# Optimization experiments

Hardware: AMD Instinct MI355X
Metric: run time of the kernel (lower is better)

## Reference

```python
import jax, jax.numpy as jnp
import numpy as np

ALPHA = 0.2  # leaky relu slope
NEG = -9e15


def setup_inputs() -> dict:
    key = jax.random.key(0)
    k1, k2, k3, k4 = jax.random.split(key, 4)
    B, N, Fin, Fout = 16, 2048, 256, 256
    h = jax.random.normal(k1, (B, N, Fin), dtype=jnp.float32)
    adj = jax.random.randint(k2, (B, N, N), 0, 2, dtype=jnp.int32)
    # xavier_uniform with gain 1.414 on [B, Fin, Fout] (fan over last two dims)
    limW = 1.414 * np.sqrt(6.0 / (Fin + Fout))
    W = jax.random.uniform(k3, (B, Fin, Fout), minval=-limW, maxval=limW, dtype=jnp.float32)
    lima = 1.414 * np.sqrt(6.0 / (2 * Fout + 1))
    a = jax.random.uniform(k4, (B, 2 * Fout, 1), minval=-lima, maxval=lima, dtype=jnp.float32)
    return {"h": h, "adj": adj, "W": W, "a": a}


def reference(h, adj, W, a):
    Fout = W.shape[-1]
    Wh = jnp.einsum('bnf,bfo->bno', h, W)                 # [B,N,Fout]
    Wh1 = jnp.einsum('bno,bo->bn', Wh, a[:, :Fout, 0])    # [B,N]
    Wh2 = jnp.einsum('bno,bo->bn', Wh, a[:, Fout:, 0])    # [B,N]
    e = Wh1[:, :, None] + Wh2[:, None, :]                 # [B,N,N]
    e = jnp.where(e > 0, e, ALPHA * e)                    # leaky relu
    att = jnp.where(adj > 0, e, NEG)
    att = jax.nn.softmax(att, axis=1)                     # NOTE: dim=1 as in source
    # dropout: eval mode -> identity
    h_prime = jnp.einsum('bij,bjo->bio', att, Wh)         # [B,N,Fout]
    return jax.nn.elu(h_prime)                            # concat=True
```

## Files before the change

kernel.cpp:

```cpp
#include <hip/hip_runtime.h>
#include <hip/hip_bf16.h>

typedef unsigned short u16;
typedef unsigned long long u64;
typedef __attribute__((ext_vector_type(8))) short bf16x8;
typedef __attribute__((ext_vector_type(4))) float f32x4;

#define NB 16
#define NN 2048
#define FF 256
#define LOG2E 1.4426950408889634f

__device__ __forceinline__ u16 f2bf(float x) {
    union { float f; unsigned u; } v; v.f = x;
    unsigned r = v.u + 0x7fffu + ((v.u >> 16) & 1u);
    return (u16)(r >> 16);
}

#define GLD_LDS(g, l) __builtin_amdgcn_global_load_lds((const __attribute__((address_space(1))) void*)(g), (__attribute__((address_space(3))) void*)(l), 16, 0, 0)

__global__ __launch_bounds__(256) void k_prep_w(const float* __restrict__ W, const float* __restrict__ a,
                                                u16* __restrict__ WT, float* __restrict__ u1, float* __restrict__ u2) {
    int b = blockIdx.y, t = threadIdx.x;
    __shared__ float a1s[FF], a2s[FF];
    a1s[t] = a[b*2*FF + t];
    a2s[t] = a[b*2*FF + FF + t];
    __syncthreads();
    int f = blockIdx.x*64 + (t >> 2);
    int o0 = (t & 3) * 64;
    const float* wrow = W + (size_t)(b*FF + f)*FF + o0;
    u16* wtb = WT + (size_t)b*FF*FF;
    float s1 = 0.f, s2 = 0.f;
#pragma unroll
    for (int c = 0; c < 16; ++c) {
        float4 v = *(const float4*)(wrow + c*4);
        int o = o0 + c*4;
        s1 += v.x*a1s[o] + v.y*a1s[o+1] + v.z*a1s[o+2] + v.w*a1s[o+3];
        s2 += v.x*a2s[o] + v.y*a2s[o+1] + v.z*a2s[o+2] + v.w*a2s[o+3];
        wtb[(size_t)(o+0)*FF + f] = f2bf(v.x);
        wtb[(size_t)(o+1)*FF + f] = f2bf(v.y);
        wtb[(size_t)(o+2)*FF + f] = f2bf(v.z);
        wtb[(size_t)(o+3)*FF + f] = f2bf(v.w);
    }
    s1 += __shfl_xor(s1, 1); s1 += __shfl_xor(s1, 2);
    s2 += __shfl_xor(s2, 1); s2 += __shfl_xor(s2, 2);
    if ((t & 3) == 0) { u1[b*FF + f] = s1; u2[b*FF + f] = s2; }
}

__global__ __launch_bounds__(256) void k_wh(const float* __restrict__ h, const u16* __restrict__ WT,
                                            const float* __restrict__ u1, const float* __restrict__ u2,
                                            u16* __restrict__ WhT, float* __restrict__ Wh1, float* __restrict__ Wh2) {
    int bid = blockIdx.x;
    int nid = (bid & 7)*64 + (bid >> 3);
    int b  = nid >> 5;
    int i0 = (nid & 31) * 64;
    int t = threadIdx.x, lane = t & 63, wave = t >> 6;
    __shared__ alignas(16) u16 At[256*64];
    __shared__ alignas(16) u16 Bt[64*64];
    __shared__ float u1s[FF], u2s[FF];
    u1s[t] = u1[b*FF + t];
    u2s[t] = u2[b*FF + t];

    const u16*   WTb = WT + (size_t)b*FF*FF;
    const float* hb  = h + ((size_t)b*NN + i0)*FF;
    int r = t >> 2, q = t & 3, kq = q*16;

    f32x4 acc[4][4];
#pragma unroll
    for (int x = 0; x < 4; ++x)
#pragma unroll
        for (int y = 0; y < 4; ++y) acc[x][y] = (f32x4)0.f;
    float s1 = 0.f, s2 = 0.f;
    __syncthreads();

#pragma unroll 1
    for (int kk = 0; kk < 4; ++kk) {
        int k0 = kk*64;
#pragma unroll
        for (int is = 0; is < 8; ++is) {
            int s = is*256 + t;
            int row = s >> 3, jbp = s & 7;
            int jbl = jbp ^ (row & 7);
            GLD_LDS(WTb + (size_t)row*FF + k0 + jbl*8, &At[s*8]);
        }
        {
            const float* hp = hb + (size_t)r*FF + k0 + kq;
            float4 f0 = *(const float4*)(hp + 0);
            float4 f1 = *(const float4*)(hp + 4);
            float4 f2 = *(const float4*)(hp + 8);
            float4 f3 = *(const float4*)(hp + 12);
            float fv[16] = {f0.x,f0.y,f0.z,f0.w, f1.x,f1.y,f1.z,f1.w,
                            f2.x,f2.y,f2.z,f2.w, f3.x,f3.y,f3.z,f3.w};
            union { u16 u[16]; bf16x8 v[2]; } cv;
#pragma unroll
            for (int e = 0; e < 16; ++e) {
                int kidx = k0 + kq + e;
                s1 += fv[e]*u1s[kidx];
                s2 += fv[e]*u2s[kidx];
                cv.u[e] = f2bf(fv[e]);
            }
            int rx = r & 7;
            *(bf16x8*)&Bt[r*64 + ((q*2 + 0) ^ rx)*8] = cv.v[0];
            *(bf16x8*)&Bt[r*64 + ((q*2 + 1) ^ rx)*8] = cv.v[1];
        }
        __syncthreads();
#pragma unroll
        for (int kc = 0; kc < 2; ++kc) {
            int jl = kc*4 + (lane >> 4);
            bf16x8 af[4], bfr[4];
#pragma unroll
            for (int mi = 0; mi < 4; ++mi) {
                int rr2 = wave*64 + mi*16 + (lane & 15);
                af[mi] = *(const bf16x8*)&At[rr2*64 + ((jl ^ (rr2 & 7))*8)];
            }
#pragma unroll
            for (int ni = 0; ni < 4; ++ni) {
                int rr2 = ni*16 + (lane & 15);
                bfr[ni] = *(const bf16x8*)&Bt[rr2*64 + ((jl ^ (rr2 & 7))*8)];
            }
#pragma unroll
            for (int mi = 0; mi < 4; ++mi)
#pragma unroll
                for (int ni = 0; ni < 4; ++ni)
                    acc[mi][ni] = __builtin_amdgcn_mfma_f32_16x16x32_bf16(af[mi], bfr[ni], acc[mi][ni], 0, 0, 0);
        }
        __syncthreads();
    }
    s1 += __shfl_xor(s1, 1); s1 += __shfl_xor(s1, 2);
    s2 += __shfl_xor(s2, 1); s2 += __shfl_xor(s2, 2);
    if (q == 0) { Wh1[b*NN + i0 + r] = s1*LOG2E; Wh2[b*NN + i0 + r] = s2*LOG2E; }

    u16* Wo = WhT + (size_t)b*FF*NN;
#pragma unroll
    for (int mi = 0; mi < 4; ++mi)
#pragma unroll
        for (int ni = 0; ni < 4; ++ni) {
            int i = i0 + ni*16 + (lane & 15);
#pragma unroll
            for (int rr = 0; rr < 4; ++rr) {
                int o = wave*64 + mi*16 + (lane >> 4)*4 + rr;
                Wo[(size_t)o*NN + i] = f2bf(acc[mi][ni][rr]);
            }
        }
}

__global__ __launch_bounds__(256) void k_colsum(const int* __restrict__ adj, const float* __restrict__ Wh1,
                                                const float* __restrict__ Wh2, float* __restrict__ pS,
                                                u64* __restrict__ packed) {
    int b = blockIdx.z, ic = blockIdx.y, jt = blockIdx.x;
    int t = threadIdx.x, lane = t & 63, wave = t >> 6;
    __shared__ float wh1s[128];
    int ibase = ic*128;
    if (t < 128) wh1s[t] = Wh1[b*NN + ibase + t];
    __syncthreads();
    int j = jt*256 + wave*16 + (lane & 15) + (lane >> 4)*64;
    float wh2j = Wh2[b*NN + j];
    const int* acol = adj + (size_t)b*NN*NN + (size_t)ibase*NN + j;
    u64* prow = packed + ((size_t)(b*NN + ibase))*32 + wave*8 + jt;
    float s = 0.f;
#pragma unroll 1
    for (int ii = 0; ii < 128; ii += 16) {
        int v[16];
#pragma unroll
        for (int rr = 0; rr < 16; ++rr) v[rr] = acol[(size_t)(ii + rr)*NN];
#pragma unroll
        for (int rr = 0; rr < 16; ++rr) {
            bool p = v[rr] > 0;
            u64 m = __ballot(p);
            if (lane == 0) prow[(size_t)(ii + rr)*32] = m;
            float tt = wh1s[ii + rr] + wh2j;
            float lr = fmaxf(tt, 0.2f*tt);
            float e = __builtin_amdgcn_exp2f(lr);
            s += p ? e : 0.f;
        }
    }
    pS[((size_t)(b*16 + ic))*NN + j] = s;
}

__global__ __launch_bounds__(512, 1) void k_gemm3(const u16* __restrict__ WhT, const u64* __restrict__ packed,
                                                  const float* __restrict__ Wh1, const float* __restrict__ Wh2,
                                                  const float* __restrict__ pS, float* __restrict__ out) {
    int bid = blockIdx.x;
    int nid = (bid & 7)*32 + (bid >> 3);
    int b  = nid >> 4;
    int i0 = (nid & 15) * 128;
    int t = threadIdx.x, lane = t & 63, wave = t >> 6;
    int wm = wave >> 2, wn = wave & 3;
    __shared__ alignas(16) u16 At[2][128*64];
    __shared__ alignas(16) u16 Bt[3][256*64];
    __shared__ float wh2s[NN];
    __shared__ float e2ps[NN];
    __shared__ float e2ns[NN];
    __shared__ unsigned zlut[4];

    const u16* Wo = WhT + (size_t)b*FF*NN;
    int rA = t >> 2, qA = t & 3;
    const u64* pkrow = packed + ((size_t)b*NN + i0 + rA)*32 + qA*8;

    float wh1r = Wh1[b*NN + i0 + rA];
    float e1p = __builtin_amdgcn_exp2f(wh1r);
    float e1n = __builtin_amdgcn_exp2f(0.2f*wh1r);

#pragma unroll
    for (int c = 0; c < 4; ++c) {
        int idx = c*512 + t;
        float w2 = Wh2[b*NN + idx];
        float s = 0.f;
#pragma unroll
        for (int cc = 0; cc < 16; ++cc) s += pS[((size_t)(b*16 + cc))*NN + idx];
        float inv = (s > 0.f) ? 1.0f/s : 0.0f;
        wh2s[idx] = w2;
        e2ps[idx] = __builtin_amdgcn_exp2f(w2) * inv;
        e2ns[idx] = __builtin_amdgcn_exp2f(0.2f*w2) * inv;
    }
    if (t < 4) zlut[t] = ((t & 1) ? 0xFFFFu : 0u) | ((t & 2) ? 0xFFFF0000u : 0u);

    auto stageB = [&](int kk, int bbuf) {
        int k0 = kk*64;
#pragma unroll
        for (int is = 0; is < 4; ++is) {
            int s = is*512 + t;
            int row = s >> 3, jbp = s & 7;
            int jbl = jbp ^ (row & 7);
            GLD_LDS(Wo + (size_t)row*NN + k0 + jbl*8, &Bt[bbuf][s*8]);
        }
    };
    auto genA = [&](int g, int abuf, unsigned mask16) {
        int rx = rA & 7;
#pragma unroll
        for (int hf = 0; hf < 2; ++hf) {
            union { unsigned w[4]; bf16x8 v; } ob;
#pragma unroll
            for (int q4 = 0; q4 < 2; ++q4) {
                int jb = g*64 + qA*16 + hf*8 + q4*4;
                float4 w2 = *(const float4*)&wh2s[jb];
                float4 tp = *(const float4*)&e2ps[jb];
                float4 tn = *(const float4*)&e2ns[jb];
                float xs[4] = {w2.x, w2.y, w2.z, w2.w};
                float ps[4] = {tp.x, tp.y, tp.z, tp.w};
                float ns[4] = {tn.x, tn.y, tn.z, tn.w};
                float pe[4];
#pragma unroll
                for (int e = 0; e < 4; ++e) {
                    float tt = wh1r + xs[e];
                    bool pos = tt > 0.f;
                    pe[e] = (pos ? e1p : e1n) * (pos ? ps[e] : ns[e]);
                }
                unsigned bits = mask16 >> (hf*8 + q4*4);
#pragma unroll
                for (int p = 0; p < 2; ++p) {
                    unsigned w;
                    asm("v_cvt_pk_bf16_f32 %0, %1, %2" : "=v"(w) : "v"(pe[2*p]), "v"(pe[2*p+1]));
                    ob.w[q4*2 + p] = w & zlut[(bits >> (2*p)) & 3];
                }
            }
            *(bf16x8*)&At[abuf][rA*64 + (((qA*2 + hf) ^ rx)*8)] = ob.v;
        }
    };

#define MM(mi, ni, af, bf) acc[mi][ni] = __builtin_amdgcn_mfma_f32_16x16x32_bf16(af, bf, acc[mi][ni], 0, 0, 0)

    f32x4 acc[4][4];
#pragma unroll
    for (int x = 0; x < 4; ++x)
#pragma unroll
        for (int y = 0; y < 4; ++y) acc[x][y] = (f32x4)0.f;

    u64 mcur = pkrow[0];
    u64 mnext = pkrow[1];
    __syncthreads();
    stageB(0, 0);
    stageB(1, 1);
    genA(0, 0, (unsigned)(mcur & 0xffffu));
    asm volatile("s_waitcnt vmcnt(4) lgkmcnt(0)" ::: "memory");
    __builtin_amdgcn_s_barrier();

    int ibr = 0, ibs = 2;
#pragma unroll 1
    for (int kk = 0; kk < 32; ++kk) {
        int g = kk + 1;
        if (g < 32 && (g & 3) == 0) {
            mcur = mnext;
            if (g + 4 < 32) mnext = pkrow[(g + 4) >> 2];
        }
        if (kk + 2 < 32) stageB(kk + 2, ibs);
        if (g < 32) {
            unsigned mask16 = (unsigned)((mcur >> ((g & 3)*16)) & 0xffffu);
            genA(g, g & 1, mask16);
        }
        int ra = kk & 1;
#pragma unroll
        for (int kc = 0; kc < 2; ++kc) {
            int jl = kc*4 + (lane >> 4);
            bf16x8 af[2], af2[2], bfr[4];
#pragma unroll
            for (int mi = 0; mi < 2; ++mi) {
                int rr2 = wm*64 + mi*16 + (lane & 15);
                af[mi] = *(const bf16x8*)&At[ra][rr2*64 + ((jl ^ (rr2 & 7))*8)];
            }
#pragma unroll
            for (int ni = 0; ni < 4; ++ni) {
                int rr2 = wn*64 + ni*16 + (lane & 15);
                bfr[ni] = *(const bf16x8*)&Bt[ibr][rr2*64 + ((jl ^ (rr2 & 7))*8)];
            }
            __builtin_amdgcn_s_setprio(1);
            MM(0,0,af[0],bfr[0]); MM(0,1,af[0],bfr[1]); MM(0,2,af[0],bfr[2]); MM(0,3,af[0],bfr[3]);
            MM(1,0,af[1],bfr[0]); MM(1,1,af[1],bfr[1]); MM(1,2,af[1],bfr[2]); MM(1,3,af[1],bfr[3]);
            __builtin_amdgcn_s_setprio(0);
#pragma unroll
            for (int mi = 2; mi < 4; ++mi) {
                int rr2 = wm*64 + mi*16 + (lane & 15);
                af2[mi-2] = *(const bf16x8*)&At[ra][rr2*64 + ((jl ^ (rr2 & 7))*8)];
            }
            __builtin_amdgcn_s_setprio(1);
            MM(2,0,af2[0],bfr[0]); MM(2,1,af2[0],bfr[1]); MM(2,2,af2[0],bfr[2]); MM(2,3,af2[0],bfr[3]);
            MM(3,0,af2[1],bfr[0]); MM(3,1,af2[1],bfr[1]); MM(3,2,af2[1],bfr[2]); MM(3,3,af2[1],bfr[3]);
            __builtin_amdgcn_s_setprio(0);
        }
        if (kk < 30) asm volatile("s_waitcnt vmcnt(4) lgkmcnt(0)" ::: "memory");
        else         asm volatile("s_waitcnt vmcnt(0) lgkmcnt(0)" ::: "memory");
        __builtin_amdgcn_s_barrier();
        ibr = (ibr + 1 == 3) ? 0 : ibr + 1;
        ibs = (ibs + 1 == 3) ? 0 : ibs + 1;
    }
#undef MM

    float* ob2 = out + ((size_t)b*NN)*FF;
#pragma unroll
    for (int mi = 0; mi < 4; ++mi)
#pragma unroll
        for (int ni = 0; ni < 4; ++ni) {
            int o = wn*64 + ni*16 + (lane & 15);
#pragma unroll
            for (int rr = 0; rr < 4; ++rr) {
                int i = i0 + wm*64 + mi*16 + (lane >> 4)*4 + rr;
                float x = acc[mi][ni][rr];
                float y = (x > 0.f) ? x : (__builtin_amdgcn_exp2f(x*LOG2E) - 1.f);
                ob2[(size_t)i*FF + o] = y;
            }
        }
}

extern "C" void kernel_launch(void* const* d_in, const int* in_sizes, int n_in,
                              void* d_out, int out_size, void* d_ws, size_t ws_size,
                              hipStream_t stream) {
    const float* h   = (const float*)d_in[0];
    const int*   adj = (const int*)d_in[1];
    const float* W   = (const float*)d_in[2];
    const float* a   = (const float*)d_in[3];
    float* out = (float*)d_out;

    char* w = (char*)d_ws;
    const size_t MB = 1u << 20;
    u16* WT   = (u16*)(w + 0);
    u16* WhT  = (u16*)(w + 2*MB);
    u64* packed = (u64*)(w + 18*MB);
    float* pS  = (float*)(w + 26*MB);
    float* Wh1 = (float*)(w + 28*MB);
    float* Wh2 = (float*)(w + 28*MB + 131072);
    float* u1  = (float*)(w + 28*MB + 2*131072);
    float* u2  = (float*)(w + 28*MB + 2*131072 + 16384);

    k_prep_w<<<dim3(4, 16), 256, 0, stream>>>(W, a, WT, u1, u2);
    k_wh<<<dim3(512), 256, 0, stream>>>(h, WT, u1, u2, WhT, Wh1, Wh2);
    k_colsum<<<dim3(8, 16, 16), 256, 0, stream>>>(adj, Wh1, Wh2, pS, packed);
    k_gemm3<<<dim3(256), 512, 0, stream>>>(WhT, packed, Wh1, Wh2, pS, out);
}
```

Baseline: 155.8 us.

## Rewrite adjacency pass as row-wise vectorized pack with factored exponentials

Replaces the column-strided k_colsum, which used a ballot per row, with k_pack. Each thread in k_pack reads 8 contiguous adjacency ints per row through int4 loads and builds the bitmask bytes in shared memory. The per-element exp2 is factored into exp2(Wh1)*exp2(Wh2), split by the sign of the leaky-relu argument. The packed-mask layout is transposed to [b][chunk][row], and the partial column sums grow to 32 chunks. k_gemm3 is adjusted to fetch one mask word per k-step, prefetched two steps ahead. The goal is more coalesced streaming of the large adj tensor and fewer transcendentals, at the cost of a smaller grid and a larger pS reduction.

```diff
diff --git a/kernel.cpp b/kernel.cpp
--- a/kernel.cpp
+++ b/kernel.cpp
@@ -144,37 +144,77 @@
         }
 }
 
-__global__ __launch_bounds__(256) void k_colsum(const int* __restrict__ adj, const float* __restrict__ Wh1,
-                                                const float* __restrict__ Wh2, float* __restrict__ pS,
-                                                u64* __restrict__ packed) {
-    int b = blockIdx.z, ic = blockIdx.y, jt = blockIdx.x;
-    int t = threadIdx.x, lane = t & 63, wave = t >> 6;
-    __shared__ float wh1s[128];
-    int ibase = ic*128;
-    if (t < 128) wh1s[t] = Wh1[b*NN + ibase + t];
+__global__ __launch_bounds__(256) void k_pack(const int* __restrict__ adj, const float* __restrict__ Wh1,
+                                              const float* __restrict__ Wh2, float* __restrict__ pS,
+                                              u64* __restrict__ packed) {
+    int b = blockIdx.y, ic = blockIdx.x;
+    int t = threadIdx.x;
+    __shared__ float wh1s[64], e1ps[64], e1ns[64];
+    __shared__ unsigned char mk[64][256];
+    int ibase = ic*64;
+    if (t < 64) {
+        float w1 = Wh1[b*NN + ibase + t];
+        wh1s[t] = w1;
+        e1ps[t] = __builtin_amdgcn_exp2f(w1);
+        e1ns[t] = __builtin_amdgcn_exp2f(0.2f*w1);
+    }
+    float w2[8];
+    {
+        float4 a0 = *(const float4*)(Wh2 + b*NN + t*8);
+        float4 a1 = *(const float4*)(Wh2 + b*NN + t*8 + 4);
+        w2[0]=a0.x; w2[1]=a0.y; w2[2]=a0.z; w2[3]=a0.w;
+        w2[4]=a1.x; w2[5]=a1.y; w2[6]=a1.z; w2[7]=a1.w;
+    }
     __syncthreads();
-    int j = jt*256 + wave*16 + (lane & 15) + (lane >> 4)*64;
-    float wh2j = Wh2[b*NN + j];
-    const int* acol = adj + (size_t)b*NN*NN + (size_t)ibase*NN + j;
-    u64* prow = packed + ((size_t)(b*NN + ibase))*32 + wave*8 + jt;
-    float s = 0.f;
+    const int* abase = adj + ((size_t)(b*NN + ibase))*NN + t*8;
+    float sp[8] = {0.f,0.f,0.f,0.f,0.f,0.f,0.f,0.f};
+    float sn[8] = {0.f,0.f,0.f,0.f,0.f,0.f,0.f,0.f};
 #pragma unroll 1
-    for (int ii = 0; ii < 128; ii += 16) {
-        int v[16];
-#pragma unroll
-        for (int rr = 0; rr < 16; ++rr) v[rr] = acol[(size_t)(ii + rr)*NN];
-#pragma unroll
-        for (int rr = 0; rr < 16; ++rr) {
-            bool p = v[rr] > 0;
-            u64 m = __ballot(p);
-            if (lane == 0) prow[(size_t)(ii + rr)*32] = m;
-            float tt = wh1s[ii + rr] + wh2j;
-            float lr = fmaxf(tt, 0.2f*tt);
-            float e = __builtin_amdgcn_exp2f(lr);
-            s += p ? e : 0.f;
-        }
-    }
-    pS[((size_t)(b*16 + ic))*NN + j] = s;
+    for (int r4 = 0; r4 < 16; ++r4) {
+        int4 v[4][2];
+#pragma unroll
+        for (int k = 0; k < 4; ++k) {
+            v[k][0] = *(const int4*)(abase + (size_t)(r4*4 + k)*NN);
+            v[k][1] = *(const int4*)(abase + (size_t)(r4*4 + k)*NN + 4);
+        }
+#pragma unroll
+        for (int k = 0; k < 4; ++k) {
+            int row = r4*4 + k;
+            float w1 = wh1s[row], ep = e1ps[row], en = e1ns[row];
+            int a[8] = {v[k][0].x, v[k][0].y, v[k][0].z, v[k][0].w,
+                        v[k][1].x, v[k][1].y, v[k][1].z, v[k][1].w};
+            unsigned bits = 0;
+#pragma unroll
+            for (int e = 0; e < 8; ++e) {
+                bool bit = a[e] > 0;
+                bool pos = (w1 + w2[e]) > 0.f;
+                bits |= bit ? (1u << e) : 0u;
+                sp[e] += (bit && pos)  ? ep : 0.f;
+                sn[e] += (bit && !pos) ? en : 0.f;
+            }
+            mk[row][t] = (unsigned char)bits;
+        }
+    }
+    __syncthreads();
+    {
+        int g = t >> 3, r0 = (t & 7)*8;
+        u64* dst = packed + ((size_t)(b*32 + g))*NN + ibase + r0;
+#pragma unroll
+        for (int k = 0; k < 8; ++k)
+            dst[k] = *(const u64*)&mk[r0 + k][g*8];
+    }
+    {
+        float o8[8];
+#pragma unroll
+        for (int e = 0; e < 8; ++e) {
+            float E2p = __builtin_amdgcn_exp2f(w2[e]);
+            float E2n = __builtin_amdgcn_exp2f(0.2f*w2[e]);
+            o8[e] = E2p*sp[e] + E2n*sn[e];
+        }
+        float4* po = (float4*)(pS + ((size_t)(b*32 + ic))*NN + t*8);
+        po[0] = make_float4(o8[0],o8[1],o8[2],o8[3]);
+        po[1] = make_float4(o8[4],o8[5],o8[6],o8[7]);
+    }
 }
 
 __global__ __launch_bounds__(512, 1) void k_gemm3(const u16* __restrict__ WhT, const u64* __restrict__ packed,
@@ -195,7 +235,7 @@
 
     const u16* Wo = WhT + (size_t)b*FF*NN;
     int rA = t >> 2, qA = t & 3;
-    const u64* pkrow = packed + ((size_t)b*NN + i0 + rA)*32 + qA*8;
+    const u64* pkbase = packed + (size_t)b*32*NN + i0 + rA;
 
     float wh1r = Wh1[b*NN + i0 + rA];
     float e1p = __builtin_amdgcn_exp2f(wh1r);
@@ -207,7 +247,7 @@
         float w2 = Wh2[b*NN + idx];
         float s = 0.f;
 #pragma unroll
-        for (int cc = 0; cc < 16; ++cc) s += pS[((size_t)(b*16 + cc))*NN + idx];
+        for (int cc = 0; cc < 32; ++cc) s += pS[((size_t)(b*32 + cc))*NN + idx];
         float inv = (s > 0.f) ? 1.0f/s : 0.0f;
         wh2s[idx] = w2;
         e2ps[idx] = __builtin_amdgcn_exp2f(w2) * inv;
@@ -266,12 +306,12 @@
 #pragma unroll
         for (int y = 0; y < 4; ++y) acc[x][y] = (f32x4)0.f;
 
-    u64 mcur = pkrow[0];
-    u64 mnext = pkrow[1];
+    u64 mcur = pkbase[0];
+    u64 mnext = pkbase[NN];
     __syncthreads();
     stageB(0, 0);
     stageB(1, 1);
-    genA(0, 0, (unsigned)(mcur & 0xffffu));
+    genA(0, 0, (unsigned)((mcur >> (qA*16)) & 0xffffu));
     asm volatile("s_waitcnt vmcnt(4) lgkmcnt(0)" ::: "memory");
     __builtin_amdgcn_s_barrier();
 
@@ -279,15 +319,11 @@
 #pragma unroll 1
     for (int kk = 0; kk < 32; ++kk) {
         int g = kk + 1;
-        if (g < 32 && (g & 3) == 0) {
-            mcur = mnext;
-            if (g + 4 < 32) mnext = pkrow[(g + 4) >> 2];
-        }
-        if (kk + 2 < 32) stageB(kk + 2, ibs);
-        if (g < 32) {
-            unsigned mask16 = (unsigned)((mcur >> ((g & 3)*16)) & 0xffffu);
-            genA(g, g & 1, mask16);
-        }
+        bool havef = (kk + 2 < 32);
+        u64 mfut = 0;
+        if (havef) mfut = pkbase[(size_t)(kk + 2)*NN];
+        if (havef) stageB(kk + 2, ibs);
+        if (g < 32) genA(g, g & 1, (unsigned)((mnext >> (qA*16)) & 0xffffu));
         int ra = kk & 1;
 #pragma unroll
         for (int kc = 0; kc < 2; ++kc) {
@@ -320,6 +356,7 @@
         if (kk < 30) asm volatile("s_waitcnt vmcnt(4) lgkmcnt(0)" ::: "memory");
         else         asm volatile("s_waitcnt vmcnt(0) lgkmcnt(0)" ::: "memory");
         __builtin_amdgcn_s_barrier();
+        if (havef) mnext = mfut;
         ibr = (ibr + 1 == 3) ? 0 : ibr + 1;
         ibs = (ibs + 1 == 3) ? 0 : ibs + 1;
     }
@@ -356,13 +393,13 @@
     u16* WhT  = (u16*)(w + 2*MB);
     u64* packed = (u64*)(w + 18*MB);
     float* pS  = (float*)(w + 26*MB);
-    float* Wh1 = (float*)(w + 28*MB);
-    float* Wh2 = (float*)(w + 28*MB + 131072);
-    float* u1  = (float*)(w + 28*MB + 2*131072);
-    float* u2  = (float*)(w + 28*MB + 2*131072 + 16384);
+    float* Wh1 = (float*)(w + 34*MB);
+    float* Wh2 = (float*)(w + 34*MB + 131072);
+    float* u1  = (float*)(w + 34*MB + 2*131072);
+    float* u2  = (float*)(w + 34*MB + 2*131072 + 16384);
 
     k_prep_w<<<dim3(4, 16), 256, 0, stream>>>(W, a, WT, u1, u2);
     k_wh<<<dim3(512), 256, 0, stream>>>(h, WT, u1, u2, WhT, Wh1, Wh2);
-    k_colsum<<<dim3(8, 16, 16), 256, 0, stream>>>(adj, Wh1, Wh2, pS, packed);
+    k_pack<<<dim3(32, 16), 256, 0, stream>>>(adj, Wh1, Wh2, pS, packed);
     k_gemm3<<<dim3(256), 512, 0, stream>>>(WhT, packed, Wh1, Wh2, pS, out);
 }
```

Result: faster. 149.4 us (-4.1%).
